# Optimization experiments

Hardware: AMD Instinct MI355X
Metric: run time of the kernel (lower is better)

## Reference

```python
import jax, jax.numpy as jnp
import numpy as np

D = 768
H = 16
DK = D // H
DFF = 3072
POOL = 100
NCLS = 7
EPS = 1e-6


def layer_norm(x, a, b):
    # torch: (x - mean) / (std + eps), std unbiased (ddof=1)
    mean = jnp.mean(x, axis=-1, keepdims=True)
    var = jnp.sum((x - mean) ** 2, axis=-1, keepdims=True) / (x.shape[-1] - 1)
    return a * (x - mean) / (jnp.sqrt(var) + EPS) + b


def mha(x, Wq, bq, Wk, bk, Wv, bv, Wo, bo):
    B, S, _ = x.shape
    def split(h):
        return h.reshape(B, S, H, DK).transpose(0, 2, 1, 3)  # [B,H,S,DK]
    q = split(x @ Wq + bq)
    k = split(x @ Wk + bk)
    v = split(x @ Wv + bv)
    scores = jnp.einsum('bhqd,bhkd->bhqk', q, k) / jnp.sqrt(jnp.float32(DK))
    p = jax.nn.softmax(scores, axis=-1)
    o = jnp.einsum('bhqk,bhkd->bhqd', p, v)
    o = o.transpose(0, 2, 1, 3).reshape(B, S, D)
    return o @ Wo + bo


def setup_inputs() -> dict:
    key = jax.random.key(0)
    ks = jax.random.split(key, 24)
    B, S = 8, 1023
    s = 0.02
    inp = {
        'text_features': jax.random.normal(ks[0], (B, S, D), jnp.float32),
        'prompt_pool': jax.random.normal(ks[1], (POOL, D), jnp.float32),
        'cls_token': jax.random.normal(ks[2], (1, 1, D), jnp.float32),
        'Wq': jax.random.normal(ks[3], (D, D), jnp.float32) * s,
        'bq': jnp.zeros((D,), jnp.float32),
        'Wk': jax.random.normal(ks[4], (D, D), jnp.float32) * s,
        'bk': jnp.zeros((D,), jnp.float32),
        'Wv': jax.random.normal(ks[5], (D, D), jnp.float32) * s,
        'bv': jnp.zeros((D,), jnp.float32),
        'Wo': jax.random.normal(ks[6], (D, D), jnp.float32) * s,
        'bo': jnp.zeros((D,), jnp.float32),
        'ln1_a': jnp.ones((D,), jnp.float32),
        'ln1_b': jnp.zeros((D,), jnp.float32),
        'ln2_a': jnp.ones((D,), jnp.float32),
        'ln2_b': jnp.zeros((D,), jnp.float32),
        'W1': jax.random.normal(ks[7], (D, DFF), jnp.float32) * s,
        'b1': jnp.zeros((DFF,), jnp.float32),
        'W2': jax.random.normal(ks[8], (DFF, D), jnp.float32) * s,
        'b2': jnp.zeros((D,), jnp.float32),
        'lnf_a': jnp.ones((D,), jnp.float32),
        'lnf_b': jnp.zeros((D,), jnp.float32),
        'Wpool': jax.random.normal(ks[9], (D, POOL), jnp.float32) * s,
        'bpool': jnp.zeros((POOL,), jnp.float32),
        'Wcls': jax.random.normal(ks[10], (D, NCLS), jnp.float32) * s,
        'bcls': jnp.zeros((NCLS,), jnp.float32),
    }
    return inp


def reference(text_features, prompt_pool, cls_token, Wq, bq, Wk, bk, Wv, bv, Wo, bo,
              ln1_a, ln1_b, ln2_a, ln2_b, W1, b1, W2, b2, lnf_a, lnf_b,
              Wpool, bpool, Wcls, bcls):
    B = text_features.shape[0]
    x = jnp.concatenate([jnp.broadcast_to(cls_token, (B, 1, D)), text_features], axis=1)
    # EncoderLayer (N=1), dropout in eval mode (identity)
    x = x + mha(layer_norm(x, ln1_a, ln1_b), Wq, bq, Wk, bk, Wv, bv, Wo, bo)
    h = layer_norm(x, ln2_a, ln2_b)
    x = x + (jax.nn.relu(h @ W1 + b1) @ W2 + b2)
    x = layer_norm(x, lnf_a, lnf_b)
    cls = x[:, 0, :]  # [B, D]
    probabilities = jax.nn.softmax(cls @ Wpool + bpool, axis=1)  # [B, POOL]
    class_logits = cls @ Wcls + bcls  # [B, NCLS]
    class_probs = jax.nn.softmax(class_logits, axis=1)
    entropy = -jnp.sum(class_probs * jnp.log(class_probs + 1e-9), axis=1)
    max_entropy = jnp.log(jnp.float32(7.0))
    norm_ent = entropy / max_entropy
    adjusted_k = jnp.clip(jnp.floor(1.0 + norm_ent * (POOL - 1)).astype(jnp.int32), 1, POOL)  # [B]
    # full descending top-k (jit-friendly: pad to POOL instead of data-dependent max_k)
    _, top_idx = jax.lax.top_k(probabilities, POOL)  # [B, POOL]
    gathered = prompt_pool[top_idx]  # [B, POOL, D]
    keep = (jnp.arange(POOL)[None, :] < adjusted_k[:, None]).astype(prompt_pool.dtype)
    selected_prompts = gathered * keep[:, :, None]
    return (selected_prompts, class_logits)
```

## Files before the change

### kernel.cpp

```cpp
#include <hip/hip_runtime.h>


#define OUT_CLS_OFF 614400

__device__ __forceinline__ float bsum256(float v, float* red) {
    int lane = threadIdx.x & 63, w = threadIdx.x >> 6;
#pragma unroll
    for (int off = 1; off < 64; off <<= 1) v += __shfl_xor(v, off);
    __syncthreads();
    if (lane == 0) red[w] = v;
    __syncthreads();
    return red[0] + red[1] + red[2] + red[3];
}
__device__ __forceinline__ float bmax256(float v, float* red) {
    int lane = threadIdx.x & 63, w = threadIdx.x >> 6;
#pragma unroll
    for (int off = 1; off < 64; off <<= 1) v = fmaxf(v, __shfl_xor(v, off));
    __syncthreads();
    if (lane == 0) red[w] = v;
    __syncthreads();
    return fmaxf(fmaxf(red[0], red[1]), fmaxf(red[2], red[3]));
}

__global__ __launch_bounds__(256) void prep_a(
    const float* __restrict__ clsT, const float* __restrict__ ga,
    const float* __restrict__ gb, const float* __restrict__ Wq,
    const float* __restrict__ bq, const float* __restrict__ Wk,
    float* __restrict__ q0, float* __restrict__ colw)
{
    __shared__ float ys[768];
    __shared__ float red[4];
    __shared__ float4 partA[16][17];
    __shared__ float4 partB[16][17];
    int t = threadIdx.x;
    if (blockIdx.x < 12) {
        float a0 = clsT[t], a1 = clsT[t + 256], a2 = clsT[t + 512];
        float mean = bsum256(a0 + a1 + a2, red) * (1.0f / 768.0f);
        float d0 = a0 - mean, d1 = a1 - mean, d2 = a2 - mean;
        float var = bsum256(d0 * d0 + d1 * d1 + d2 * d2, red) * (1.0f / 767.0f);
        float den = sqrtf(var) + 1e-6f;
        ys[t]       = (ga[t] * d0) / den + gb[t];
        ys[t + 256] = (ga[t + 256] * d1) / den + gb[t + 256];
        ys[t + 512] = (ga[t + 512] * d2) / den + gb[t + 512];
        __syncthreads();
        int c = blockIdx.x * 64 + (t & 15) * 4;
        int kq = t >> 4;
        float4 acc = {0.f, 0.f, 0.f, 0.f};
#pragma unroll 8
        for (int i = 0; i < 48; ++i) {
            int k = kq * 48 + i;
            float4 w = *(const float4*)&Wq[(size_t)k * 768 + c];
            float y = ys[k];
            acc.x = fmaf(y, w.x, acc.x); acc.y = fmaf(y, w.y, acc.y);
            acc.z = fmaf(y, w.z, acc.z); acc.w = fmaf(y, w.w, acc.w);
        }
        partA[kq][t & 15] = acc;
        __syncthreads();
        if (t < 16) {
            float4 s = {0.f, 0.f, 0.f, 0.f};
#pragma unroll
            for (int i = 0; i < 16; ++i) {
                float4 v = partA[i][t];
                s.x += v.x; s.y += v.y; s.z += v.z; s.w += v.w;
            }
            int cc = blockIdx.x * 64 + t * 4;
            float4 b4 = *(const float4*)&bq[cc];
            q0[cc] = s.x + b4.x; q0[cc + 1] = s.y + b4.y;
            q0[cc + 2] = s.z + b4.z; q0[cc + 3] = s.w + b4.w;
        }
    } else {
        int c = (blockIdx.x - 12) * 64 + (t & 15) * 4;
        int kq = t >> 4;
        float4 aa = {0.f, 0.f, 0.f, 0.f}, ab = {0.f, 0.f, 0.f, 0.f};
#pragma unroll 8
        for (int i = 0; i < 48; ++i) {
            int k = kq * 48 + i;
            float4 w = *(const float4*)&Wk[(size_t)k * 768 + c];
            float g = ga[k], h = gb[k];
            aa.x = fmaf(g, w.x, aa.x); aa.y = fmaf(g, w.y, aa.y);
            aa.z = fmaf(g, w.z, aa.z); aa.w = fmaf(g, w.w, aa.w);
            ab.x = fmaf(h, w.x, ab.x); ab.y = fmaf(h, w.y, ab.y);
            ab.z = fmaf(h, w.z, ab.z); ab.w = fmaf(h, w.w, ab.w);
        }
        partA[kq][t & 15] = aa;
        partB[kq][t & 15] = ab;
        __syncthreads();
        if (t < 16) {
            float4 sa = {0.f, 0.f, 0.f, 0.f}, sb = {0.f, 0.f, 0.f, 0.f};
#pragma unroll
            for (int i = 0; i < 16; ++i) {
                float4 va = partA[i][t], vb = partB[i][t];
                sa.x += va.x; sa.y += va.y; sa.z += va.z; sa.w += va.w;
                sb.x += vb.x; sb.y += vb.y; sb.z += vb.z; sb.w += vb.w;
            }
            int cc = (blockIdx.x - 12) * 64 + t * 4;
            *(float4*)&colw[cc] = sa;
            *(float4*)&colw[768 + cc] = sb;
        }
    }
}

__global__ __launch_bounds__(256) void prep_b(
    const float* __restrict__ Wk, const float* __restrict__ bk,
    const float* __restrict__ q0, const float* __restrict__ colw,
    float* __restrict__ wkqc)
{
    __shared__ float qs[768];
    int t = threadIdx.x;
    qs[t] = q0[t]; qs[t + 256] = q0[t + 256]; qs[t + 512] = q0[t + 512];
    __syncthreads();
    const float invs = 0.14433756729740643f;
    int kl = t >> 4, h = t & 15;
    int k = blockIdx.x * 16 + kl;
    const float* wr = Wk + (size_t)k * 768 + h * 48;
    const float* qh = qs + h * 48;
    float a = 0.f;
#pragma unroll
    for (int d = 0; d < 48; d += 4) {
        float4 w = *(const float4*)&wr[d];
        a += w.x * qh[d] + w.y * qh[d + 1] + w.z * qh[d + 2] + w.w * qh[d + 3];
    }
    wkqc[k * 16 + h] = a * invs;
    if (blockIdx.x == 0 && t < 16) {
        float cd = 0.f, sa = 0.f, sb = 0.f;
        for (int d = 0; d < 48; ++d) {
            int dd = t * 48 + d;
            cd = fmaf(bk[dd], qs[dd], cd);
            sa = fmaf(colw[dd], qs[dd], sa);
            sb = fmaf(colw[768 + dd], qs[dd], sb);
        }
        wkqc[12304 + t] = sa * invs;
        wkqc[12320 + t] = sb * invs + cd * invs;
    }
}

__global__ __launch_bounds__(256) void ln_scores(
    const float* __restrict__ tf, const float* __restrict__ clsT,
    const float* __restrict__ ga, const float* __restrict__ wkqc,
    float* __restrict__ sc, float2* __restrict__ stats)
{
    __shared__ float tr[256][17];
    __shared__ float partw[4][16];
    __shared__ float red[2][4][2];
    int t = threadIdx.x;
    int l = t & 63, w = t >> 6;

    float wk0[16], wk1[16], wk2[16];
    {
        const float4* p0 = (const float4*)(wkqc + t * 16);
        const float4* p1 = (const float4*)(wkqc + (t + 256) * 16);
        const float4* p2 = (const float4*)(wkqc + (t + 512) * 16);
#pragma unroll
        for (int q = 0; q < 4; ++q) {
            float4 v0 = p0[q], v1 = p1[q], v2 = p2[q];
            wk0[q * 4] = v0.x; wk0[q * 4 + 1] = v0.y; wk0[q * 4 + 2] = v0.z; wk0[q * 4 + 3] = v0.w;
            wk1[q * 4] = v1.x; wk1[q * 4 + 1] = v1.y; wk1[q * 4 + 2] = v1.z; wk1[q * 4 + 3] = v1.w;
            wk2[q * 4] = v2.x; wk2[q * 4 + 1] = v2.y; wk2[q * 4 + 2] = v2.z; wk2[q * 4 + 3] = v2.w;
        }
    }
    float ga0 = ga[t], ga1 = ga[t + 256], ga2 = ga[t + 512];
    float Sg = wkqc[12304 + (t & 15)];
    float Cg = wkqc[12320 + (t & 15)];

    int r0 = blockIdx.x * 8;
    for (int r = 0; r < 8; ++r) {
        int row = r0 + r;
        int b = row >> 10, j = row & 1023;
        const float* src = j ? (tf + ((size_t)b * 1023 + (j - 1)) * 768) : clsT;
        float x0 = src[t], x1 = src[t + 256], x2 = src[t + 512];
        float s1 = x0 + x1 + x2;
        float s2 = fmaf(x0, x0, fmaf(x1, x1, x2 * x2));
        float g0 = ga0 * x0, g1 = ga1 * x1, g2 = ga2 * x2;
        float dt[16];
#pragma unroll
        for (int h = 0; h < 16; ++h)
            dt[h] = fmaf(g0, wk0[h], fmaf(g1, wk1[h], g2 * wk2[h]));
#pragma unroll
        for (int off = 1; off < 64; off <<= 1) {
            s1 += __shfl_xor(s1, off);
            s2 += __shfl_xor(s2, off);
        }
        if (l == 0) { red[r & 1][w][0] = s1; red[r & 1][w][1] = s2; }
#pragma unroll
        for (int h = 0; h < 16; ++h) tr[t][h] = dt[h];
        __syncthreads();
        int hh = t & 15, ch = t >> 4;
        float v = 0.f;
#pragma unroll
        for (int i = 0; i < 16; ++i) v += tr[ch * 16 + i][hh];
        v += __shfl_xor(v, 16);
        v += __shfl_xor(v, 32);
        if (l < 16) partw[w][l] = v;
        __syncthreads();
        if (t < 16) {
            float dtot = partw[0][t] + partw[1][t] + partw[2][t] + partw[3][t];
            float s1t = red[r & 1][0][0] + red[r & 1][1][0] + red[r & 1][2][0] + red[r & 1][3][0];
            float s2t = red[r & 1][0][1] + red[r & 1][1][1] + red[r & 1][2][1] + red[r & 1][3][1];
            float mean = s1t * (1.0f / 768.0f);
            float var = (s2t - mean * s1t) * (1.0f / 767.0f);
            float rden = 1.0f / (sqrtf(var) + 1e-6f);
            float sv = rden * (dtot - mean * Sg) + Cg;
            sc[(((size_t)b * 16 + t) << 10) + j] = sv;
            if (t == 0) stats[row] = make_float2(mean, rden);
        }
    }
}

__global__ __launch_bounds__(256) void softmax_q(
    const float* __restrict__ sc, const float2* __restrict__ stats,
    float* __restrict__ qb, float* __restrict__ c1w)
{
    __shared__ float red[4];
    int bh = blockIdx.x, t = threadIdx.x;
    int b = bh >> 4;
    const float4* s4 = (const float4*)(sc + ((size_t)bh << 10));
    float4 v = s4[t];
    float m = fmaxf(fmaxf(v.x, v.y), fmaxf(v.z, v.w));
    float M = bmax256(m, red);
    float e0 = expf(v.x - M), e1 = expf(v.y - M), e2 = expf(v.z - M), e3 = expf(v.w - M);
    float Z = bsum256(e0 + e1 + e2 + e3, red);
    float2 st0 = stats[(b << 10) + 4 * t];
    float2 st1 = stats[(b << 10) + 4 * t + 1];
    float2 st2 = stats[(b << 10) + 4 * t + 2];
    float2 st3 = stats[(b << 10) + 4 * t + 3];
    float q0v = (e0 / Z) * st0.y, q1v = (e1 / Z) * st1.y;
    float q2v = (e2 / Z) * st2.y, q3v = (e3 / Z) * st3.y;
    float c1t = bsum256(q0v * st0.x + q1v * st1.x + q2v * st2.x + q3v * st3.x, red);
    float4 o4; o4.x = q0v; o4.y = q1v; o4.z = q2v; o4.w = q3v;
    ((float4*)(qb + ((size_t)bh << 10)))[t] = o4;
    if (t == 0) c1w[bh] = c1t;
}

__global__ __launch_bounds__(256) void upart_k(
    const float* __restrict__ tf, const float* __restrict__ clsT,
    const float* __restrict__ qb, float* __restrict__ up)
{
    __shared__ float qs_s[16][32];
    int b = blockIdx.x & 7, jc = blockIdx.x >> 3;
    int t = threadIdx.x;
    if (t < 128) {
        int h = t >> 3, j4 = (t & 7) * 4;
        float4 pv = *(const float4*)(qb + (((size_t)b * 16 + h) << 10) + jc * 32 + j4);
        qs_s[h][j4] = pv.x; qs_s[h][j4 + 1] = pv.y;
        qs_s[h][j4 + 2] = pv.z; qs_s[h][j4 + 3] = pv.w;
    }
    __syncthreads();
    float acc[16][3];
#pragma unroll
    for (int h = 0; h < 16; ++h) { acc[h][0] = 0.f; acc[h][1] = 0.f; acc[h][2] = 0.f; }
    int j0 = jc * 32;
    const float* sp0 = j0 ? (tf + ((size_t)b * 1023 + (j0 - 1)) * 768) : clsT;
    float nx0 = sp0[t], nx1 = sp0[t + 256], nx2 = sp0[t + 512];
    for (int jj = 0; jj < 32; ++jj) {
        float x0 = nx0, x1 = nx1, x2 = nx2;
        if (jj < 31) {
            const float* sp = tf + ((size_t)b * 1023 + j0 + jj) * 768;
            nx0 = sp[t]; nx1 = sp[t + 256]; nx2 = sp[t + 512];
        }
#pragma unroll
        for (int h = 0; h < 16; ++h) {
            float qh = qs_s[h][jj];
            acc[h][0] = fmaf(qh, x0, acc[h][0]);
            acc[h][1] = fmaf(qh, x1, acc[h][1]);
            acc[h][2] = fmaf(qh, x2, acc[h][2]);
        }
    }
    float* o = up + (((size_t)b * 32 + jc) * 16) * 768;
#pragma unroll
    for (int h = 0; h < 16; ++h) {
        o[h * 768 + t] = acc[h][0];
        o[h * 768 + t + 256] = acc[h][1];
        o[h * 768 + t + 512] = acc[h][2];
    }
}

__global__ __launch_bounds__(256) void o0_k(
    const float* __restrict__ up, const float* __restrict__ c1w,
    const float* __restrict__ ga, const float* __restrict__ gb,
    const float* __restrict__ Wv, const float* __restrict__ bv,
    float* __restrict__ o0)
{
    __shared__ float us[768];
    __shared__ float part[4][64];
    int h = blockIdx.x, b = blockIdx.y, t = threadIdx.x;
    float s0 = 0.f, s1 = 0.f, s2 = 0.f;
#pragma unroll 8
    for (int jc = 0; jc < 32; ++jc) {
        const float* q = up + (((size_t)b * 32 + jc) * 16 + h) * 768;
        s0 += q[t]; s1 += q[t + 256]; s2 += q[t + 512];
    }
    float c1 = c1w[b * 16 + h];
    us[t]       = ga[t] * (s0 - c1) + gb[t];
    us[t + 256] = ga[t + 256] * (s1 - c1) + gb[t + 256];
    us[t + 512] = ga[t + 512] * (s2 - c1) + gb[t + 512];
    __syncthreads();
    int dd = t & 63, kg = t >> 6;
    float a = 0.f;
    if (dd < 48) {
#pragma unroll 8
        for (int i = 0; i < 192; ++i) {
            int k = kg * 192 + i;
            a = fmaf(us[k], Wv[(size_t)k * 768 + h * 48 + dd], a);
        }
    }
    part[kg][dd] = a;
    __syncthreads();
    if (t < 48)
        o0[(size_t)b * 768 + h * 48 + t] =
            part[0][t] + part[1][t] + part[2][t] + part[3][t] + bv[h * 48 + t];
}

__global__ __launch_bounds__(256) void x2_k(
    const float* __restrict__ o0, const float* __restrict__ Wo,
    const float* __restrict__ bo, const float* __restrict__ clsT,
    float* __restrict__ x2w)
{
    __shared__ float ys[768];
    __shared__ float4 part[16][17];
    int b = blockIdx.y, t = threadIdx.x;
    const float* xr = o0 + (size_t)b * 768;
    ys[t] = xr[t]; ys[t + 256] = xr[t + 256]; ys[t + 512] = xr[t + 512];
    __syncthreads();
    int c = blockIdx.x * 64 + (t & 15) * 4;
    int kq = t >> 4;
    float4 acc = {0.f, 0.f, 0.f, 0.f};
#pragma unroll 8
    for (int i = 0; i < 48; ++i) {
        int k = kq * 48 + i;
        float4 w = *(const float4*)&Wo[(size_t)k * 768 + c];
        float y = ys[k];
        acc.x = fmaf(y, w.x, acc.x); acc.y = fmaf(y, w.y, acc.y);
        acc.z = fmaf(y, w.z, acc.z); acc.w = fmaf(y, w.w, acc.w);
    }
    part[kq][t & 15] = acc;
    __syncthreads();
    if (t < 16) {
        float4 s = {0.f, 0.f, 0.f, 0.f};
#pragma unroll
        for (int i = 0; i < 16; ++i) {
            float4 v = part[i][t];
            s.x += v.x; s.y += v.y; s.z += v.z; s.w += v.w;
        }
        int cc = blockIdx.x * 64 + t * 4;
        float4 b4 = *(const float4*)&bo[cc];
        float4 r4 = *(const float4*)&clsT[cc];
        float* o = x2w + (size_t)b * 768 + cc;
        o[0] = s.x + b4.x + r4.x; o[1] = s.y + b4.y + r4.y;
        o[2] = s.z + b4.z + r4.z; o[3] = s.w + b4.w + r4.w;
    }
}

__global__ __launch_bounds__(256) void f1_k(
    const float* __restrict__ x2w, const float* __restrict__ ga,
    const float* __restrict__ gb, const float* __restrict__ W1,
    const float* __restrict__ b1, float* __restrict__ f1w)
{
    __shared__ float ys[768];
    __shared__ float red[4];
    __shared__ float4 part[8][33];
    int b = blockIdx.y, t = threadIdx.x;
    const float* xr = x2w + (size_t)b * 768;
    float a0 = xr[t], a1 = xr[t + 256], a2 = xr[t + 512];
    float mean = bsum256(a0 + a1 + a2, red) * (1.0f / 768.0f);
    float d0 = a0 - mean, d1 = a1 - mean, d2 = a2 - mean;
    float var = bsum256(d0 * d0 + d1 * d1 + d2 * d2, red) * (1.0f / 767.0f);
    float den = sqrtf(var) + 1e-6f;
    ys[t]       = (ga[t] * d0) / den + gb[t];
    ys[t + 256] = (ga[t + 256] * d1) / den + gb[t + 256];
    ys[t + 512] = (ga[t + 512] * d2) / den + gb[t + 512];
    __syncthreads();
    int c = blockIdx.x * 128 + (t & 31) * 4;
    int kq = t >> 5;
    float4 acc = {0.f, 0.f, 0.f, 0.f};
#pragma unroll 8
    for (int i = 0; i < 96; ++i) {
        int k = kq * 96 + i;
        float4 w = *(const float4*)&W1[(size_t)k * 3072 + c];
        float y = ys[k];
        acc.x = fmaf(y, w.x, acc.x); acc.y = fmaf(y, w.y, acc.y);
        acc.z = fmaf(y, w.z, acc.z); acc.w = fmaf(y, w.w, acc.w);
    }
    part[kq][t & 31] = acc;
    __syncthreads();
    if (t < 32) {
        float4 s = {0.f, 0.f, 0.f, 0.f};
#pragma unroll
        for (int i = 0; i < 8; ++i) {
            float4 v = part[i][t];
            s.x += v.x; s.y += v.y; s.z += v.z; s.w += v.w;
        }
        int cc = blockIdx.x * 128 + t * 4;
        float4 b4 = *(const float4*)&b1[cc];
        float* o = f1w + (size_t)b * 3072 + cc;
        o[0] = fmaxf(s.x + b4.x, 0.f); o[1] = fmaxf(s.y + b4.y, 0.f);
        o[2] = fmaxf(s.z + b4.z, 0.f); o[3] = fmaxf(s.w + b4.w, 0.f);
    }
}

__global__ __launch_bounds__(256) void x3_k(
    const float* __restrict__ f1w, const float* __restrict__ W2,
    const float* __restrict__ b2, const float* __restrict__ x2w,
    float* __restrict__ x3w)
{
    __shared__ float ys[3072];
    __shared__ float4 part[16][17];
    int b = blockIdx.y, t = threadIdx.x;
    const float* xr = f1w + (size_t)b * 3072;
    for (int i = t; i < 3072; i += 256) ys[i] = xr[i];
    __syncthreads();
    int c = blockIdx.x * 64 + (t & 15) * 4;
    int kq = t >> 4;
    float4 acc = {0.f, 0.f, 0.f, 0.f};
#pragma unroll 8
    for (int i = 0; i < 192; ++i) {
        int k = kq * 192 + i;
        float4 w = *(const float4*)&W2[(size_t)k * 768 + c];
        float y = ys[k];
        acc.x = fmaf(y, w.x, acc.x); acc.y = fmaf(y, w.y, acc.y);
        acc.z = fmaf(y, w.z, acc.z); acc.w = fmaf(y, w.w, acc.w);
    }
    part[kq][t & 15] = acc;
    __syncthreads();
    if (t < 16) {
        float4 s = {0.f, 0.f, 0.f, 0.f};
#pragma unroll
        for (int i = 0; i < 16; ++i) {
            float4 v = part[i][t];
            s.x += v.x; s.y += v.y; s.z += v.z; s.w += v.w;
        }
        int cc = blockIdx.x * 64 + t * 4;
        float4 b4 = *(const float4*)&b2[cc];
        const float* x2r = x2w + (size_t)b * 768 + cc;
        float* o = x3w + (size_t)b * 768 + cc;
        o[0] = x2r[0] + s.x + b4.x; o[1] = x2r[1] + s.y + b4.y;
        o[2] = x2r[2] + s.z + b4.z; o[3] = x2r[3] + s.w + b4.w;
    }
}

__global__ __launch_bounds__(256) void logits_part(
    const float* __restrict__ x3w, const float* __restrict__ ga,
    const float* __restrict__ gb, const float* __restrict__ Wpool,
    const float* __restrict__ Wcls, double* __restrict__ lp)
{
    __shared__ float ys[768];
    __shared__ float red[4];
    int kg = blockIdx.x, b = blockIdx.y, t = threadIdx.x;
    const float* xr = x3w + (size_t)b * 768;
    float a0 = xr[t], a1 = xr[t + 256], a2 = xr[t + 512];
    float mean = bsum256(a0 + a1 + a2, red) * (1.0f / 768.0f);
    float d0 = a0 - mean, d1 = a1 - mean, d2 = a2 - mean;
    float var = bsum256(d0 * d0 + d1 * d1 + d2 * d2, red) * (1.0f / 767.0f);
    float den = sqrtf(var) + 1e-6f;
    ys[t]       = (ga[t] * d0) / den + gb[t];
    ys[t + 256] = (ga[t + 256] * d1) / den + gb[t + 256];
    ys[t + 512] = (ga[t + 512] * d2) / den + gb[t + 512];
    __syncthreads();
    int kbase = kg * 96;
    if (t < 100) {
        double a = 0.0;
#pragma unroll 8
        for (int i = 0; i < 96; ++i) {
            int k = kbase + i;
            a = fma((double)ys[k], (double)Wpool[k * 100 + t], a);
        }
        lp[((size_t)b * 8 + kg) * 112 + t] = a;
    } else if (t < 107) {
        int c = t - 100;
        double a = 0.0;
#pragma unroll 8
        for (int i = 0; i < 96; ++i) {
            int k = kbase + i;
            a = fma((double)ys[k], (double)Wcls[k * 7 + c], a);
        }
        lp[((size_t)b * 8 + kg) * 112 + t] = a;
    }
}

__global__ __launch_bounds__(128) void head_decide(
    const double* __restrict__ lp, const float* __restrict__ bpool,
    const float* __restrict__ bcls, float* __restrict__ out,
    int* __restrict__ topw, int* __restrict__ kkw)
{
    __shared__ double sP[100];
    __shared__ double sC7[7];
    int b = blockIdx.x, t = threadIdx.x;
    if (t < 107) {
        double a = (t < 100) ? (double)bpool[t] : (double)bcls[t - 100];
#pragma unroll
        for (int kg = 0; kg < 8; ++kg) a += lp[((size_t)b * 8 + kg) * 112 + t];
        if (t < 100) sP[t] = a;
        else {
            sC7[t - 100] = a;
            out[OUT_CLS_OFF + b * 7 + (t - 100)] = (float)a;
        }
    }
    __syncthreads();
    double mx = sP[0];
    for (int j = 1; j < 100; ++j) mx = fmax(mx, sP[j]);
    double e = (t < 100) ? exp(sP[t] - mx) : 0.0;
    __syncthreads();
    if (t < 100) sP[t] = e;
    __syncthreads();
    double zs = 0.0;
    for (int j = 0; j < 100; ++j) zs += sP[j];
    __syncthreads();
    if (t < 100) sP[t] = e / zs;
    __syncthreads();
    if (t == 0) {
        double m7 = sC7[0];
        for (int j = 1; j < 7; ++j) m7 = fmax(m7, sC7[j]);
        double es[7]; double z = 0.0;
        for (int j = 0; j < 7; ++j) { es[j] = exp(sC7[j] - m7); z += es[j]; }
        double ent = 0.0;
        for (int j = 0; j < 7; ++j) { double pr = es[j] / z; ent -= pr * log(pr + 1e-9); }
        double ne = ent / log(7.0);
        int kk = (int)floor(1.0 + ne * 99.0);
        kkw[b] = kk < 1 ? 1 : (kk > 100 ? 100 : kk);
    }
    if (t < 100) {
        double pi = sP[t];
        int r = 0;
        for (int j = 0; j < 100; ++j) {
            double pj = sP[j];
            r += (pj > pi) || (pj == pi && j < t);
        }
        topw[b * 100 + r] = t;
    }
}

__global__ __launch_bounds__(192) void gather_k(
    const float* __restrict__ pool, const int* __restrict__ topw,
    const int* __restrict__ kkw, float* __restrict__ out)
{
    int r = blockIdx.x, b = blockIdx.y, t = threadIdx.x;
    int idx = topw[b * 100 + r];
    bool keep = r < kkw[b];
    const float4* src = (const float4*)(pool + (size_t)idx * 768);
    float4* dst = (float4*)(out + (size_t)b * 76800 + (size_t)r * 768);
    float4 z = {0.f, 0.f, 0.f, 0.f};
    dst[t] = keep ? src[t] : z;
}

extern "C" void kernel_launch(void* const* d_in, const int* in_sizes, int n_in,
                              void* d_out, int out_size, void* d_ws, size_t ws_size,
                              hipStream_t stream) {
    (void)in_sizes; (void)n_in; (void)out_size; (void)ws_size;
    const float* tf    = (const float*)d_in[0];
    const float* pool  = (const float*)d_in[1];
    const float* clsT  = (const float*)d_in[2];
    const float* Wq    = (const float*)d_in[3];
    const float* bq    = (const float*)d_in[4];
    const float* Wk    = (const float*)d_in[5];
    const float* bk    = (const float*)d_in[6];
    const float* Wv    = (const float*)d_in[7];
    const float* bv    = (const float*)d_in[8];
    const float* Wo    = (const float*)d_in[9];
    const float* bo    = (const float*)d_in[10];
    const float* ln1a  = (const float*)d_in[11];
    const float* ln1b  = (const float*)d_in[12];
    const float* ln2a  = (const float*)d_in[13];
    const float* ln2b  = (const float*)d_in[14];
    const float* W1    = (const float*)d_in[15];
    const float* b1    = (const float*)d_in[16];
    const float* W2    = (const float*)d_in[17];
    const float* b2    = (const float*)d_in[18];
    const float* lnfa  = (const float*)d_in[19];
    const float* lnfb  = (const float*)d_in[20];
    const float* Wpool = (const float*)d_in[21];
    const float* bpool = (const float*)d_in[22];
    const float* Wcls  = (const float*)d_in[23];
    const float* bcls  = (const float*)d_in[24];
    float* out = (float*)d_out;
    char* ws = (char*)d_ws;

    float*  sc    = (float*)(ws + 0);
    float*  qb    = (float*)(ws + 524288);
    float2* stats = (float2*)(ws + 1048576);
    float*  wkqc  = (float*)(ws + 1114112);
    float*  q0    = (float*)(ws + 1163520);
    float*  colw  = (float*)(ws + 1166592);
    float*  c1w   = (float*)(ws + 1172736);
    float*  up    = (float*)(ws + 1173248);
    float*  o0    = (float*)(ws + 13756160);
    float*  x2w   = (float*)(ws + 13780736);
    float*  f1w   = (float*)(ws + 13805312);
    float*  x3w   = (float*)(ws + 13903616);
    int*    topw  = (int*)(ws + 13928192);
    int*    kkw   = (int*)(ws + 13931392);
    double* lp    = (double*)(ws + 13931424);

    prep_a<<<24, 256, 0, stream>>>(clsT, ln1a, ln1b, Wq, bq, Wk, q0, colw);
    prep_b<<<48, 256, 0, stream>>>(Wk, bk, q0, colw, wkqc);
    ln_scores<<<1024, 256, 0, stream>>>(tf, clsT, ln1a, wkqc, sc, stats);
    softmax_q<<<128, 256, 0, stream>>>(sc, stats, qb, c1w);
    upart_k<<<256, 256, 0, stream>>>(tf, clsT, qb, up);
    o0_k<<<dim3(16, 8), 256, 0, stream>>>(up, c1w, ln1a, ln1b, Wv, bv, o0);
    x2_k<<<dim3(12, 8), 256, 0, stream>>>(o0, Wo, bo, clsT, x2w);
    f1_k<<<dim3(24, 8), 256, 0, stream>>>(x2w, ln2a, ln2b, W1, b1, f1w);
    x3_k<<<dim3(12, 8), 256, 0, stream>>>(f1w, W2, b2, x2w, x3w);
    logits_part<<<dim3(8, 8), 256, 0, stream>>>(x3w, lnfa, lnfb, Wpool, Wcls, lp);
    head_decide<<<8, 128, 0, stream>>>(lp, bpool, bcls, out, topw, kkw);
    gather_k<<<dim3(100, 8), 192, 0, stream>>>(pool, topw, kkw, out);
}
```

Before: 107.1 us.

## Fold softmax into scores/upart and fuse head decision via last-block atomic

Drops the separate softmax kernel. Scores are written as unnormalised exp(s)*rden, and upart now also emits per-chunk partial normalisers and mean-correction sums, which o0_k reduces to apply 1/Z. The head_decide kernel is merged into logits_part through an atomic counter, so the last block for each batch does the decision work. ln_scores also prefetches the next row. Skipping the max subtraction risks exp overflow if scores grow large, and the atomic counter adds a fence plus counter reset in prep_a.

Result: slower. 110.2 us (+2.9%).

```diff
diff --git a/kernel.cpp b/kernel.cpp
--- a/kernel.cpp
+++ b/kernel.cpp
@@ -11,28 +11,20 @@
     if (lane == 0) red[w] = v;
     __syncthreads();
     return red[0] + red[1] + red[2] + red[3];
-}
-__device__ __forceinline__ float bmax256(float v, float* red) {
-    int lane = threadIdx.x & 63, w = threadIdx.x >> 6;
-#pragma unroll
-    for (int off = 1; off < 64; off <<= 1) v = fmaxf(v, __shfl_xor(v, off));
-    __syncthreads();
-    if (lane == 0) red[w] = v;
-    __syncthreads();
-    return fmaxf(fmaxf(red[0], red[1]), fmaxf(red[2], red[3]));
 }
 
 __global__ __launch_bounds__(256) void prep_a(
     const float* __restrict__ clsT, const float* __restrict__ ga,
     const float* __restrict__ gb, const float* __restrict__ Wq,
     const float* __restrict__ bq, const float* __restrict__ Wk,
-    float* __restrict__ q0, float* __restrict__ colw)
+    float* __restrict__ q0, float* __restrict__ colw, int* __restrict__ cnts)
 {
     __shared__ float ys[768];
     __shared__ float red[4];
     __shared__ float4 partA[16][17];
     __shared__ float4 partB[16][17];
     int t = threadIdx.x;
+    if (blockIdx.x == 0 && t < 16) cnts[t] = 0;
     if (blockIdx.x < 12) {
         float a0 = clsT[t], a1 = clsT[t + 256], a2 = clsT[t + 512];
         float mean = bsum256(a0 + a1 + a2, red) * (1.0f / 768.0f);
@@ -163,14 +155,19 @@
     float Cg = wkqc[12320 + (t & 15)];
 
     int r0 = blockIdx.x * 8;
+    int b = r0 >> 10, j0 = r0 & 1023;
+    const float* src0 = j0 ? (tf + ((size_t)b * 1023 + (j0 - 1)) * 768) : clsT;
+    float x0 = src0[t], x1 = src0[t + 256], x2 = src0[t + 512];
     for (int r = 0; r < 8; ++r) {
-        int row = r0 + r;
-        int b = row >> 10, j = row & 1023;
-        const float* src = j ? (tf + ((size_t)b * 1023 + (j - 1)) * 768) : clsT;
-        float x0 = src[t], x1 = src[t + 256], x2 = src[t + 512];
-        float s1 = x0 + x1 + x2;
-        float s2 = fmaf(x0, x0, fmaf(x1, x1, x2 * x2));
-        float g0 = ga0 * x0, g1 = ga1 * x1, g2 = ga2 * x2;
+        int j = j0 + r;
+        float cx0 = x0, cx1 = x1, cx2 = x2;
+        if (r < 7) {
+            const float* sp = tf + ((size_t)b * 1023 + j) * 768;
+            x0 = sp[t]; x1 = sp[t + 256]; x2 = sp[t + 512];
+        }
+        float s1 = cx0 + cx1 + cx2;
+        float s2 = fmaf(cx0, cx0, fmaf(cx1, cx1, cx2 * cx2));
+        float g0 = ga0 * cx0, g1 = ga1 * cx1, g2 = ga2 * cx2;
         float dt[16];
 #pragma unroll
         for (int h = 0; h < 16; ++h)
@@ -200,49 +197,28 @@
             float var = (s2t - mean * s1t) * (1.0f / 767.0f);
             float rden = 1.0f / (sqrtf(var) + 1e-6f);
             float sv = rden * (dtot - mean * Sg) + Cg;
-            sc[(((size_t)b * 16 + t) << 10) + j] = sv;
-            if (t == 0) stats[row] = make_float2(mean, rden);
-        }
-    }
-}
-
-__global__ __launch_bounds__(256) void softmax_q(
-    const float* __restrict__ sc, const float2* __restrict__ stats,
-    float* __restrict__ qb, float* __restrict__ c1w)
-{
-    __shared__ float red[4];
-    int bh = blockIdx.x, t = threadIdx.x;
-    int b = bh >> 4;
-    const float4* s4 = (const float4*)(sc + ((size_t)bh << 10));
-    float4 v = s4[t];
-    float m = fmaxf(fmaxf(v.x, v.y), fmaxf(v.z, v.w));
-    float M = bmax256(m, red);
-    float e0 = expf(v.x - M), e1 = expf(v.y - M), e2 = expf(v.z - M), e3 = expf(v.w - M);
-    float Z = bsum256(e0 + e1 + e2 + e3, red);
-    float2 st0 = stats[(b << 10) + 4 * t];
-    float2 st1 = stats[(b << 10) + 4 * t + 1];
-    float2 st2 = stats[(b << 10) + 4 * t + 2];
-    float2 st3 = stats[(b << 10) + 4 * t + 3];
-    float q0v = (e0 / Z) * st0.y, q1v = (e1 / Z) * st1.y;
-    float q2v = (e2 / Z) * st2.y, q3v = (e3 / Z) * st3.y;
-    float c1t = bsum256(q0v * st0.x + q1v * st1.x + q2v * st2.x + q3v * st3.x, red);
-    float4 o4; o4.x = q0v; o4.y = q1v; o4.z = q2v; o4.w = q3v;
-    ((float4*)(qb + ((size_t)bh << 10)))[t] = o4;
-    if (t == 0) c1w[bh] = c1t;
+            sc[(((size_t)b * 16 + t) << 10) + j] = expf(sv) * rden;
+            if (t == 0) stats[(b << 10) + j] = make_float2(mean, rden);
+        }
+    }
 }
 
 __global__ __launch_bounds__(256) void upart_k(
     const float* __restrict__ tf, const float* __restrict__ clsT,
-    const float* __restrict__ qb, float* __restrict__ up)
+    const float* __restrict__ sc, const float2* __restrict__ stats,
+    float* __restrict__ up, float* __restrict__ upz, float* __restrict__ upc1)
 {
     __shared__ float qs_s[16][32];
+    __shared__ float2 sst[32];
     int b = blockIdx.x & 7, jc = blockIdx.x >> 3;
     int t = threadIdx.x;
     if (t < 128) {
         int h = t >> 3, j4 = (t & 7) * 4;
-        float4 pv = *(const float4*)(qb + (((size_t)b * 16 + h) << 10) + jc * 32 + j4);
+        float4 pv = *(const float4*)(sc + (((size_t)b * 16 + h) << 10) + jc * 32 + j4);
         qs_s[h][j4] = pv.x; qs_s[h][j4 + 1] = pv.y;
         qs_s[h][j4 + 2] = pv.z; qs_s[h][j4 + 3] = pv.w;
+    } else if (t < 160) {
+        sst[t - 128] = stats[(b << 10) + jc * 32 + (t - 128)];
     }
     __syncthreads();
     float acc[16][3];
@@ -272,13 +248,24 @@
         o[h * 768 + t + 256] = acc[h][1];
         o[h * 768 + t + 512] = acc[h][2];
     }
+    if (t < 16) {
+        float zp = 0.f, cp = 0.f;
+        for (int jj = 0; jj < 32; ++jj) {
+            float wv = qs_s[t][jj];
+            float2 st = sst[jj];
+            zp += wv / st.y;
+            cp += wv * st.x;
+        }
+        upz[((size_t)b * 32 + jc) * 16 + t] = zp;
+        upc1[((size_t)b * 32 + jc) * 16 + t] = cp;
+    }
 }
 
 __global__ __launch_bounds__(256) void o0_k(
-    const float* __restrict__ up, const float* __restrict__ c1w,
-    const float* __restrict__ ga, const float* __restrict__ gb,
-    const float* __restrict__ Wv, const float* __restrict__ bv,
-    float* __restrict__ o0)
+    const float* __restrict__ up, const float* __restrict__ upz,
+    const float* __restrict__ upc1, const float* __restrict__ ga,
+    const float* __restrict__ gb, const float* __restrict__ Wv,
+    const float* __restrict__ bv, float* __restrict__ o0)
 {
     __shared__ float us[768];
     __shared__ float part[4][64];
@@ -289,10 +276,16 @@
         const float* q = up + (((size_t)b * 32 + jc) * 16 + h) * 768;
         s0 += q[t]; s1 += q[t + 256]; s2 += q[t + 512];
     }
-    float c1 = c1w[b * 16 + h];
-    us[t]       = ga[t] * (s0 - c1) + gb[t];
-    us[t + 256] = ga[t + 256] * (s1 - c1) + gb[t + 256];
-    us[t + 512] = ga[t + 512] * (s2 - c1) + gb[t + 512];
+    float Z = 0.f, c1r = 0.f;
+#pragma unroll 8
+    for (int jc = 0; jc < 32; ++jc) {
+        Z   += upz[((size_t)b * 32 + jc) * 16 + h];
+        c1r += upc1[((size_t)b * 32 + jc) * 16 + h];
+    }
+    float rz = 1.0f / Z;
+    us[t]       = ga[t] * ((s0 - c1r) * rz) + gb[t];
+    us[t + 256] = ga[t + 256] * ((s1 - c1r) * rz) + gb[t + 256];
+    us[t + 512] = ga[t + 512] * ((s2 - c1r) * rz) + gb[t + 512];
     __syncthreads();
     int dd = t & 63, kg = t >> 6;
     float a = 0.f;
@@ -440,10 +433,16 @@
 __global__ __launch_bounds__(256) void logits_part(
     const float* __restrict__ x3w, const float* __restrict__ ga,
     const float* __restrict__ gb, const float* __restrict__ Wpool,
-    const float* __restrict__ Wcls, double* __restrict__ lp)
+    const float* __restrict__ Wcls, double* __restrict__ lp,
+    const float* __restrict__ bpool, const float* __restrict__ bcls,
+    float* __restrict__ out, int* __restrict__ topw, int* __restrict__ kkw,
+    int* __restrict__ cnts)
 {
     __shared__ float ys[768];
     __shared__ float red[4];
+    __shared__ double sPd[100];
+    __shared__ double sC7d[7];
+    __shared__ int sOld;
     int kg = blockIdx.x, b = blockIdx.y, t = threadIdx.x;
     const float* xr = x3w + (size_t)b * 768;
     float a0 = xr[t], a1 = xr[t + 256], a2 = xr[t + 512];
@@ -474,43 +473,42 @@
         }
         lp[((size_t)b * 8 + kg) * 112 + t] = a;
     }
-}
-
-__global__ __launch_bounds__(128) void head_decide(
-    const double* __restrict__ lp, const float* __restrict__ bpool,
-    const float* __restrict__ bcls, float* __restrict__ out,
-    int* __restrict__ topw, int* __restrict__ kkw)
-{
-    __shared__ double sP[100];
-    __shared__ double sC7[7];
-    int b = blockIdx.x, t = threadIdx.x;
+
+    __syncthreads();
+    __threadfence();
+    if (t == 0)
+        sOld = __hip_atomic_fetch_add(&cnts[b], 1, __ATOMIC_ACQ_REL,
+                                      __HIP_MEMORY_SCOPE_AGENT);
+    __syncthreads();
+    if (sOld != 7) return;
+
     if (t < 107) {
         double a = (t < 100) ? (double)bpool[t] : (double)bcls[t - 100];
 #pragma unroll
-        for (int kg = 0; kg < 8; ++kg) a += lp[((size_t)b * 8 + kg) * 112 + t];
-        if (t < 100) sP[t] = a;
+        for (int g = 0; g < 8; ++g) a += lp[((size_t)b * 8 + g) * 112 + t];
+        if (t < 100) sPd[t] = a;
         else {
-            sC7[t - 100] = a;
+            sC7d[t - 100] = a;
             out[OUT_CLS_OFF + b * 7 + (t - 100)] = (float)a;
         }
     }
     __syncthreads();
-    double mx = sP[0];
-    for (int j = 1; j < 100; ++j) mx = fmax(mx, sP[j]);
-    double e = (t < 100) ? exp(sP[t] - mx) : 0.0;
-    __syncthreads();
-    if (t < 100) sP[t] = e;
+    double mx = sPd[0];
+    for (int j = 1; j < 100; ++j) mx = fmax(mx, sPd[j]);
+    double e = (t < 100) ? exp(sPd[t] - mx) : 0.0;
+    __syncthreads();
+    if (t < 100) sPd[t] = e;
     __syncthreads();
     double zs = 0.0;
-    for (int j = 0; j < 100; ++j) zs += sP[j];
-    __syncthreads();
-    if (t < 100) sP[t] = e / zs;
+    for (int j = 0; j < 100; ++j) zs += sPd[j];
+    __syncthreads();
+    if (t < 100) sPd[t] = e / zs;
     __syncthreads();
     if (t == 0) {
-        double m7 = sC7[0];
-        for (int j = 1; j < 7; ++j) m7 = fmax(m7, sC7[j]);
+        double m7 = sC7d[0];
+        for (int j = 1; j < 7; ++j) m7 = fmax(m7, sC7d[j]);
         double es[7]; double z = 0.0;
-        for (int j = 0; j < 7; ++j) { es[j] = exp(sC7[j] - m7); z += es[j]; }
+        for (int j = 0; j < 7; ++j) { es[j] = exp(sC7d[j] - m7); z += es[j]; }
         double ent = 0.0;
         for (int j = 0; j < 7; ++j) { double pr = es[j] / z; ent -= pr * log(pr + 1e-9); }
         double ne = ent / log(7.0);
@@ -518,10 +516,10 @@
         kkw[b] = kk < 1 ? 1 : (kk > 100 ? 100 : kk);
     }
     if (t < 100) {
-        double pi = sP[t];
+        double pi = sPd[t];
         int r = 0;
         for (int j = 0; j < 100; ++j) {
-            double pj = sP[j];
+            double pj = sPd[j];
             r += (pj > pi) || (pj == pi && j < t);
         }
         topw[b * 100 + r] = t;
@@ -574,31 +572,32 @@
     char* ws = (char*)d_ws;
 
     float*  sc    = (float*)(ws + 0);
-    float*  qb    = (float*)(ws + 524288);
-    float2* stats = (float2*)(ws + 1048576);
-    float*  wkqc  = (float*)(ws + 1114112);
-    float*  q0    = (float*)(ws + 1163520);
-    float*  colw  = (float*)(ws + 1166592);
-    float*  c1w   = (float*)(ws + 1172736);
-    float*  up    = (float*)(ws + 1173248);
-    float*  o0    = (float*)(ws + 13756160);
-    float*  x2w   = (float*)(ws + 13780736);
-    float*  f1w   = (float*)(ws + 13805312);
-    float*  x3w   = (float*)(ws + 13903616);
-    int*    topw  = (int*)(ws + 13928192);
-    int*    kkw   = (int*)(ws + 13931392);
-    double* lp    = (double*)(ws + 13931424);
-
-    prep_a<<<24, 256, 0, stream>>>(clsT, ln1a, ln1b, Wq, bq, Wk, q0, colw);
+    float2* stats = (float2*)(ws + 524288);
+    float*  wkqc  = (float*)(ws + 589824);
+    float*  q0    = (float*)(ws + 639232);
+    float*  colw  = (float*)(ws + 642304);
+    float*  up    = (float*)(ws + 648448);
+    float*  upz   = (float*)(ws + 13231360);
+    float*  upc1  = (float*)(ws + 13247744);
+    float*  o0    = (float*)(ws + 13264128);
+    float*  x2w   = (float*)(ws + 13288704);
+    float*  f1w   = (float*)(ws + 13313280);
+    float*  x3w   = (float*)(ws + 13411584);
+    int*    topw  = (int*)(ws + 13436160);
+    int*    kkw   = (int*)(ws + 13439360);
+    double* lp    = (double*)(ws + 13439392);
+    int*    cnts  = (int*)(ws + 13496736);
+
+    prep_a<<<24, 256, 0, stream>>>(clsT, ln1a, ln1b, Wq, bq, Wk, q0, colw, cnts);
     prep_b<<<48, 256, 0, stream>>>(Wk, bk, q0, colw, wkqc);
     ln_scores<<<1024, 256, 0, stream>>>(tf, clsT, ln1a, wkqc, sc, stats);
-    softmax_q<<<128, 256, 0, stream>>>(sc, stats, qb, c1w);
-    upart_k<<<256, 256, 0, stream>>>(tf, clsT, qb, up);
-    o0_k<<<dim3(16, 8), 256, 0, stream>>>(up, c1w, ln1a, ln1b, Wv, bv, o0);
+    upart_k<<<256, 256, 0, stream>>>(tf, clsT, sc, stats, up, upz, upc1);
+    o0_k<<<dim3(16, 8), 256, 0, stream>>>(up, upz, upc1, ln1a, ln1b, Wv, bv, o0);
     x2_k<<<dim3(12, 8), 256, 0, stream>>>(o0, Wo, bo, clsT, x2w);
     f1_k<<<dim3(24, 8), 256, 0, stream>>>(x2w, ln2a, ln2b, W1, b1, f1w);
     x3_k<<<dim3(12, 8), 256, 0, stream>>>(f1w, W2, b2, x2w, x3w);
-    logits_part<<<dim3(8, 8), 256, 0, stream>>>(x3w, lnfa, lnfb, Wpool, Wcls, lp);
-    head_decide<<<8, 128, 0, stream>>>(lp, bpool, bcls, out, topw, kkw);
+    logits_part<<<dim3(8, 8), 256, 0, stream>>>(x3w, lnfa, lnfb, Wpool, Wcls,
+                                                lp, bpool, bcls, out, topw,
+                                                kkw, cnts);
     gather_k<<<dim3(100, 8), 192, 0, stream>>>(pool, topw, kkw, out);
 }
```
